# Kernel tuning notes

Measured on AMD Instinct MI355X. Metric: run time of the kernel, lower is better.

The kernel has to match this reference:

```python
import jax
import jax.numpy as jnp
import numpy as np

IN_FEATS = 784
HIDDEN_DIM = 1024
BATCH = 1024


def setup_inputs() -> dict:
    key = jax.random.key(0)
    k_px, k_W, k_c, k_V, k_b = jax.random.split(key, 5)
    pixels = jax.random.uniform(k_px, (BATCH, IN_FEATS), dtype=jnp.float32)
    W = jax.random.normal(k_W, (HIDDEN_DIM, IN_FEATS), dtype=jnp.float32)
    c = jax.random.normal(k_c, (HIDDEN_DIM,), dtype=jnp.float32)
    V = jax.random.normal(k_V, (IN_FEATS, HIDDEN_DIM), dtype=jnp.float32)
    b = jax.random.normal(k_b, (IN_FEATS,), dtype=jnp.float32)
    return {"pixels": pixels, "W": W, "c": c, "V": V, "b": b}


def reference(pixels, W, c, V, b):
    # pixels: [B, D]; W: [H, D]; c: [H]; V: [D, H]; b: [D]
    B = pixels.shape[0]
    a0 = jnp.broadcast_to(c[None, :], (B, c.shape[0]))  # [B, H]

    def step(a, inp):
        w_col, v_row, b_i, x_i = inp  # [H], [H], [], [B]
        h = jax.nn.sigmoid(a)                     # [B, H]
        pred_i = b_i + h @ v_row                  # [B]
        a_next = a + w_col[None, :] * x_i[:, None]  # rank-1 accumulator update
        return a_next, pred_i

    xs = (W.T, V, b, pixels.T)  # each leading dim D (scan over visible units)
    _, preds = jax.lax.scan(step, a0, xs)  # preds: [D, B]
    return preds.T  # [B, D]
```

## Files before the change

### kernel.cpp

```cpp
#include <hip/hip_runtime.h>
#include <stdint.h>

#define B_ 1024
#define D_ 784
#define H_ 1024
#define BH_ (B_ * H_)
#define LOG2E 1.4426950408889634f


__device__ __forceinline__ unsigned short bf16_rne(float x) {
    unsigned b = __float_as_uint(x);
    return (unsigned short)((b + 0x7FFFu + ((b >> 16) & 1u)) >> 16);
}

__device__ __forceinline__ int seg_bound(int s) {
    const int b[7] = {0, 136, 272, 400, 528, 656, 784};
    return b[s];
}

__global__ __launch_bounds__(256) void prep(const float* __restrict__ V,
                                            const float* __restrict__ W,
                                            const float* __restrict__ px,
                                            unsigned short* __restrict__ VWb,
                                            float* __restrict__ G) {
    __shared__ float smem[32 * 33];
    const int t = threadIdx.x;

    if (blockIdx.x < 800) {
        int i0 = (blockIdx.x % 25) * 32;
        int h0 = (blockIdx.x / 25) * 32;
        int tx = t & 31, ty = t >> 5;
        int hb = h0 >> 8, hr = h0 & 255;
#pragma unroll
        for (int j = 0; j < 4; ++j) {
            int i = i0 + ty + j * 8;
            if (i < D_)
                VWb[((size_t)i * 4 + hb) * 512 + hr + tx] = bf16_rne(V[(size_t)i * H_ + h0 + tx]);
        }
#pragma unroll
        for (int j = 0; j < 4; ++j) {
            int h = h0 + ty + j * 8;
            int i = i0 + tx;
            float v = 0.f;
            if (i < D_) v = W[(size_t)h * D_ + i] * LOG2E;
            smem[(ty + j * 8) * 33 + tx] = v;
        }
        __syncthreads();
#pragma unroll
        for (int j = 0; j < 4; ++j) {
            int i = i0 + ty + j * 8;
            if (i < D_)
                VWb[((size_t)i * 4 + hb) * 512 + 256 + hr + tx] = bf16_rne(smem[tx * 33 + ty + j * 8]);
        }
    } else {
        float* xs = smem;
        float* ws = smem + 512;
        int idx = blockIdx.x - 800;
        int r   = idx >> 8;
        int b0  = (idx & 15) * 64;
        int h0  = ((idx >> 4) & 15) * 64;
        int j0s = seg_bound(r), j1s = seg_bound(r + 1);

        const int tb = t >> 4, th = t & 15;
        float acc[4][4];
#pragma unroll
        for (int bi = 0; bi < 4; ++bi)
#pragma unroll
            for (int hh = 0; hh < 4; ++hh) acc[bi][hh] = 0.f;

        const int xb = t >> 3;
        const int xj = t & 7;
        const int wh = t >> 1, wj = (t & 1) * 4;

        for (int j0 = j0s; j0 < j1s; j0 += 8) {
            float xv0 = px[(size_t)(b0 + xb) * D_ + j0 + xj];
            float xv1 = px[(size_t)(b0 + 32 + xb) * D_ + j0 + xj];
            float4 wv = make_float4(0, 0, 0, 0);
            if (t < 128) wv = *(const float4*)(W + (size_t)(h0 + wh) * D_ + j0 + wj);
            __syncthreads();
            xs[xj * 64 + xb]      = xv0;
            xs[xj * 64 + 32 + xb] = xv1;
            if (t < 128) {
                ws[(wj + 0) * 64 + wh] = wv.x * LOG2E;
                ws[(wj + 1) * 64 + wh] = wv.y * LOG2E;
                ws[(wj + 2) * 64 + wh] = wv.z * LOG2E;
                ws[(wj + 3) * 64 + wh] = wv.w * LOG2E;
            }
            __syncthreads();
#pragma unroll
            for (int jj = 0; jj < 8; ++jj) {
                float4 xq = *(float4*)&xs[jj * 64 + tb * 4];
                float4 wq = *(float4*)&ws[jj * 64 + th * 4];
                float xa[4] = {xq.x, xq.y, xq.z, xq.w};
                float wa[4] = {wq.x, wq.y, wq.z, wq.w};
#pragma unroll
                for (int bi = 0; bi < 4; ++bi)
#pragma unroll
                    for (int hh = 0; hh < 4; ++hh)
                        acc[bi][hh] = fmaf(xa[bi], wa[hh], acc[bi][hh]);
            }
        }
        float* dst = G + (size_t)r * BH_;
#pragma unroll
        for (int bi = 0; bi < 4; ++bi) {
            float4 o = make_float4(acc[bi][0], acc[bi][1], acc[bi][2], acc[bi][3]);
            *(float4*)(dst + (size_t)(b0 + tb * 4 + bi) * H_ + h0 + th * 4) = o;
        }
    }
}

template <int CTRL>
__device__ __forceinline__ float dpp_add(float p) {
    int s = __builtin_amdgcn_update_dpp(0, __float_as_int(p), CTRL, 0xf, 0xf, true);
    return p + __int_as_float(s);
}
__device__ __forceinline__ float reduce_halves(float p) {
    p = dpp_add<0x111>(p);
    p = dpp_add<0x112>(p);
    p = dpp_add<0x114>(p);
    p = dpp_add<0x118>(p);
    p = dpp_add<0x142>(p);
    return p;
}

__device__ __forceinline__ void cvt8(uint4 u, float4& a, float4& b) {
    a.x = __uint_as_float(u.x << 16);
    a.y = __uint_as_float(u.x);
    a.z = __uint_as_float(u.y << 16);
    a.w = __uint_as_float(u.y);
    b.x = __uint_as_float(u.z << 16);
    b.y = __uint_as_float(u.z);
    b.z = __uint_as_float(u.w << 16);
    b.w = __uint_as_float(u.w);
}

__global__ __launch_bounds__(256, 8) void nade_main(
    const float* __restrict__ px,
    const float* __restrict__ c,
    const unsigned short* __restrict__ VWb,
    const float* __restrict__ G,
    float* __restrict__ part)
{
    const int lane = threadIdx.x & 63;
    const int wid  = threadIdx.x >> 6;
    const int gw   = blockIdx.x * 4 + wid;
    const int s    = gw % 6;
    const int r4   = gw / 6;
    const int hb   = r4 & 3;
    const int rp   = r4 >> 2;
    const int half = lane >> 5;
    const int row  = rp * 2 + half;
    const int hl   = lane & 31;
    const int h0   = hb * 256 + hl * 8;

    const int i0s = seg_bound(s), i1s = seg_bound(s + 1);

    float A[8];
    {
        float4 c0 = *(const float4*)(c + h0);
        float4 c1 = *(const float4*)(c + h0 + 4);
        A[0] = c0.x * LOG2E; A[1] = c0.y * LOG2E; A[2] = c0.z * LOG2E; A[3] = c0.w * LOG2E;
        A[4] = c1.x * LOG2E; A[5] = c1.y * LOG2E; A[6] = c1.z * LOG2E; A[7] = c1.w * LOG2E;
        for (int r = 0; r < s; ++r) {
            const float* gp = G + (size_t)r * BH_ + (size_t)row * H_ + h0;
            float4 g0 = *(const float4*)(gp);
            float4 g1 = *(const float4*)(gp + 4);
            A[0] += g0.x; A[1] += g0.y; A[2] += g0.z; A[3] += g0.w;
            A[4] += g1.x; A[5] += g1.y; A[6] += g1.z; A[7] += g1.w;
        }
    }

    const float* xp = px + (size_t)row * D_;
    float*       pp = part + ((size_t)hb * B_ + row) * D_;
    const uint4* vw = (const uint4*)VWb + ((size_t)i0s * 4 + hb) * 64 + hl;

    auto step8 = [&A](const float4& v0, const float4& v1,
                      const float4& w0, const float4& w1, float xi) -> float {
        float va[8] = {v0.x, v0.y, v0.z, v0.w, v1.x, v1.y, v1.z, v1.w};
        float wa[8] = {w0.x, w0.y, w0.z, w0.w, w1.x, w1.y, w1.z, w1.w};
        float q[8];
#pragma unroll
        for (int k = 0; k < 8; ++k) {
            float e = __builtin_amdgcn_exp2f(fminf(15.f, -A[k]));
            q[k] = 1.f + e;
            A[k] = fmaf(wa[k], xi, A[k]);
        }
        float a01 = fmaf(va[0], q[1], va[1] * q[0]);
        float a23 = fmaf(va[2], q[3], va[3] * q[2]);
        float a45 = fmaf(va[4], q[5], va[5] * q[4]);
        float a67 = fmaf(va[6], q[7], va[7] * q[6]);
        float q01 = q[0] * q[1], q23 = q[2] * q[3];
        float q45 = q[4] * q[5], q67 = q[6] * q[7];
        float n0123 = fmaf(a01, q23, a23 * q01);
        float n4567 = fmaf(a45, q67, a67 * q45);
        float q0123 = q01 * q23, q4567 = q45 * q67;
        float r = __builtin_amdgcn_rcpf(q0123 * q4567);
        float n = fmaf(n0123, q4567, n4567 * q0123);
        return n * r;
    };

    uint4 uv = vw[0], uw = vw[32];
    vw += 256;
    float4 xq = *(const float4*)(xp + i0s);

    for (int ib = i0s; ib < i1s; ib += 4) {
        int xb = (ib + 4 < i1s) ? (ib + 4) : i0s;
        float4 xq_n = *(const float4*)(xp + xb);
        float xa[4] = {xq.x, xq.y, xq.z, xq.w};
        float pr[4];
#pragma unroll
        for (int j = 0; j < 4; ++j) {
            uint4 uvn = vw[0], uwn = vw[32];
            vw += 256;
            float4 v0, v1, w0, w1;
            cvt8(uv, v0, v1);
            cvt8(uw, w0, w1);
            float p = step8(v0, v1, w0, w1, xa[j]);
            pr[j] = reduce_halves(p);
            uv = uvn; uw = uwn;
        }
        if (hl == 31) *(float4*)(pp + ib) = make_float4(pr[0], pr[1], pr[2], pr[3]);
        xq = xq_n;
    }
}

__global__ __launch_bounds__(256) void reduce_out(const float* __restrict__ part,
                                                  const float* __restrict__ bias,
                                                  float* __restrict__ out) {
    int t = blockIdx.x * 256 + threadIdx.x;
    if (t >= B_ * (D_ / 4)) return;
    int row = t / (D_ / 4);
    int ic  = (t - row * (D_ / 4)) * 4;
    float4 acc = *(const float4*)(bias + ic);
    const float* p = part + (size_t)row * D_ + ic;
#pragma unroll
    for (int hb = 0; hb < 4; ++hb) {
        float4 v = *(const float4*)(p + (size_t)hb * B_ * D_);
        acc.x += v.x; acc.y += v.y; acc.z += v.z; acc.w += v.w;
    }
    *(float4*)(out + (size_t)row * D_ + ic) = acc;
}

extern "C" void kernel_launch(void* const* d_in, const int* in_sizes, int n_in,
                              void* d_out, int out_size, void* d_ws, size_t ws_size,
                              hipStream_t stream) {
    const float* px   = (const float*)d_in[0];
    const float* W    = (const float*)d_in[1];
    const float* c    = (const float*)d_in[2];
    const float* V    = (const float*)d_in[3];
    const float* bias = (const float*)d_in[4];
    float* out = (float*)d_out;

    unsigned short* VWb = (unsigned short*)d_ws;
    float* G    = (float*)((char*)d_ws + (size_t)788 * 4096);
    float* part = G + (size_t)5 * BH_;

    prep<<<dim3(2080), 256, 0, stream>>>(V, W, px, VWb, G);

    nade_main<<<dim3(3072), 256, 0, stream>>>(px, c, VWb, G, part);

    reduce_out<<<dim3((B_ * (D_ / 4) + 255) / 256), 256, 0, stream>>>(part, bias, out);
}
```

Measured before the change: 301.3 us.

## Fuse hidden-block reduction into main kernel via shared-memory block reduce

```diff
diff --git a/kernel.cpp b/kernel.cpp
--- a/kernel.cpp
+++ b/kernel.cpp
@@ -23,7 +23,7 @@
                                             const float* __restrict__ px,
                                             unsigned short* __restrict__ VWb,
                                             float* __restrict__ G) {
-    __shared__ float smem[32 * 33];
+    __shared__ float smem[1056];
     const int t = threadIdx.x;
 
     if (blockIdx.x < 800) {
@@ -139,19 +139,20 @@
     const float* __restrict__ c,
     const unsigned short* __restrict__ VWb,
     const float* __restrict__ G,
-    float* __restrict__ part)
+    const float* __restrict__ bias,
+    float* __restrict__ out)
 {
+    __shared__ float4 red[2][4][2];
+
     const int lane = threadIdx.x & 63;
     const int wid  = threadIdx.x >> 6;
-    const int gw   = blockIdx.x * 4 + wid;
-    const int s    = gw % 6;
-    const int r4   = gw / 6;
-    const int hb   = r4 & 3;
-    const int rp   = r4 >> 2;
+    const int bid  = blockIdx.x;
+    const int s    = bid % 6;
+    const int rp   = bid / 6;
     const int half = lane >> 5;
     const int row  = rp * 2 + half;
     const int hl   = lane & 31;
-    const int h0   = hb * 256 + hl * 8;
+    const int h0   = wid * 256 + hl * 8;
 
     const int i0s = seg_bound(s), i1s = seg_bound(s + 1);
 
@@ -171,8 +172,7 @@
     }
 
     const float* xp = px + (size_t)row * D_;
-    float*       pp = part + ((size_t)hb * B_ + row) * D_;
-    const uint4* vw = (const uint4*)VWb + ((size_t)i0s * 4 + hb) * 64 + hl;
+    const uint4* vw = (const uint4*)VWb + ((size_t)i0s * 4 + wid) * 64 + hl;
 
     auto step8 = [&A](const float4& v0, const float4& v1,
                       const float4& w0, const float4& w1, float xi) -> float {
@@ -219,26 +219,24 @@
             pr[j] = reduce_halves(p);
             uv = uvn; uw = uwn;
         }
-        if (hl == 31) *(float4*)(pp + ib) = make_float4(pr[0], pr[1], pr[2], pr[3]);
+        const int par = (ib >> 2) & 1;
+        if (hl == 31) red[par][wid][half] = make_float4(pr[0], pr[1], pr[2], pr[3]);
+        __syncthreads();
+        if (threadIdx.x < 2) {
+            float4 b4 = *(const float4*)(bias + ib);
+            float4 p0 = red[par][0][threadIdx.x];
+            float4 p1 = red[par][1][threadIdx.x];
+            float4 p2 = red[par][2][threadIdx.x];
+            float4 p3 = red[par][3][threadIdx.x];
+            float4 o;
+            o.x = b4.x + ((p0.x + p1.x) + (p2.x + p3.x));
+            o.y = b4.y + ((p0.y + p1.y) + (p2.y + p3.y));
+            o.z = b4.z + ((p0.z + p1.z) + (p2.z + p3.z));
+            o.w = b4.w + ((p0.w + p1.w) + (p2.w + p3.w));
+            *(float4*)(out + (size_t)(rp * 2 + threadIdx.x) * D_ + ib) = o;
+        }
         xq = xq_n;
     }
-}
-
-__global__ __launch_bounds__(256) void reduce_out(const float* __restrict__ part,
-                                                  const float* __restrict__ bias,
-                                                  float* __restrict__ out) {
-    int t = blockIdx.x * 256 + threadIdx.x;
-    if (t >= B_ * (D_ / 4)) return;
-    int row = t / (D_ / 4);
-    int ic  = (t - row * (D_ / 4)) * 4;
-    float4 acc = *(const float4*)(bias + ic);
-    const float* p = part + (size_t)row * D_ + ic;
-#pragma unroll
-    for (int hb = 0; hb < 4; ++hb) {
-        float4 v = *(const float4*)(p + (size_t)hb * B_ * D_);
-        acc.x += v.x; acc.y += v.y; acc.z += v.z; acc.w += v.w;
-    }
-    *(float4*)(out + (size_t)row * D_ + ic) = acc;
 }
 
 extern "C" void kernel_launch(void* const* d_in, const int* in_sizes, int n_in,
@@ -253,11 +251,8 @@
 
     unsigned short* VWb = (unsigned short*)d_ws;
     float* G    = (float*)((char*)d_ws + (size_t)788 * 4096);
-    float* part = G + (size_t)5 * BH_;
 
     prep<<<dim3(2080), 256, 0, stream>>>(V, W, px, VWb, G);
 
-    nade_main<<<dim3(3072), 256, 0, stream>>>(px, c, VWb, G, part);
-
-    reduce_out<<<dim3((B_ * (D_ / 4) + 255) / 256), 256, 0, stream>>>(part, bias, out);
-}
+    nade_main<<<dim3(3072), 256, 0, stream>>>(px, c, VWb, G, bias, out);
+}
```

Result: no change. 305.4 us (median of 2 runs) (+1.4%).
